# Performance work log

Hardware: AMD Instinct MI355X
Metric: run time of the kernel (lower is better)

Reference implementation:

```python
import jax, jax.numpy as jnp
import numpy as np

EPS = 1e-5
NEG_SLOPE = 0.2  # torch LeakyReLU default in DGCNN-style SharedMLPs


def knn_idx(p, k):
    # p: [B, 3, N]; returns idx [B, N, k] of k nearest neighbors (incl. self)
    inner = jnp.einsum('bdn,bdm->bnm', p, p)           # [B,N,N]
    sq = jnp.sum(p * p, axis=1)                         # [B,N]
    neg_dist = 2.0 * inner - sq[:, :, None] - sq[:, None, :]
    return jax.lax.top_k(neg_dist, k)[1]                # [B,N,k]


def smlp1d(x, w, b, g, bt):
    # x: [B,C,N]; 1x1 conv + BatchNorm1d (batch stats) + LeakyReLU
    y = jnp.einsum('bcn,oc->bon', x, w) + b[None, :, None]
    m = y.mean(axis=(0, 2), keepdims=True)
    v = y.var(axis=(0, 2), keepdims=True)
    y = g[None, :, None] * (y - m) * jax.lax.rsqrt(v + EPS) + bt[None, :, None]
    return jax.nn.leaky_relu(y, NEG_SLOPE)


def edgeconv(x, idx, w, b, g, bt):
    # x: [B,C,N], idx: [B,N,k] -> [B,O,N]
    B = x.shape[0]
    xT = jnp.transpose(x, (0, 2, 1))                    # [B,N,C]
    nb = xT[jnp.arange(B)[:, None, None], idx]          # [B,N,k,C] gather
    ctr = jnp.broadcast_to(xT[:, :, None, :], nb.shape)
    feat = jnp.concatenate([nb - ctr, ctr], axis=-1)    # [B,N,k,2C]
    y = jnp.einsum('bnkc,oc->bnko', feat, w) + b        # 1x1 conv2d
    m = y.mean(axis=(0, 1, 2), keepdims=True)
    v = y.var(axis=(0, 1, 2), keepdims=True)
    y = g * (y - m) * jax.lax.rsqrt(v + EPS) + bt
    y = jax.nn.leaky_relu(y, NEG_SLOPE)
    y = jnp.max(y, axis=2)                              # max over k -> [B,N,O]
    return jnp.transpose(y, (0, 2, 1))                  # [B,O,N]


def setup_inputs() -> dict:
    key = jax.random.key(0)
    ks = jax.random.split(key, 16)
    B, N, K = 2, 8192, 20
    C_in = 1024 + 3 * 64  # emb_dims + n_edgeconvs_backbone*64 = 1216
    OUT = 50

    def lin(k, o, c):
        return jax.random.normal(k, (o, c), jnp.float32) * (1.0 / np.sqrt(c))

    return {
        'x': jax.random.normal(ks[0], (B, C_in, N), jnp.float32),
        'p': jax.random.normal(ks[1], (B, 3, N), jnp.float32),
        # smlp1: 1216 -> 256
        'w1': lin(ks[2], 256, C_in), 'b1': jnp.zeros((256,), jnp.float32),
        'g1': jnp.ones((256,), jnp.float32), 'bt1': jnp.zeros((256,), jnp.float32),
        # edgeconv: 512 -> 256
        'we': lin(ks[3], 256, 512), 'be': jnp.zeros((256,), jnp.float32),
        'ge': jnp.ones((256,), jnp.float32), 'bte': jnp.zeros((256,), jnp.float32),
        # smlp2 part 1: 256 -> 256
        'w2': lin(ks[4], 256, 256), 'b2': jnp.zeros((256,), jnp.float32),
        'g2': jnp.ones((256,), jnp.float32), 'bt2': jnp.zeros((256,), jnp.float32),
        # smlp2 part 2: 256 -> 128
        'w3': lin(ks[5], 128, 256), 'b3': jnp.zeros((128,), jnp.float32),
        'g3': jnp.ones((128,), jnp.float32), 'bt3': jnp.zeros((128,), jnp.float32),
        # final conv1d: 128 -> 50
        'wf': lin(ks[6], OUT, 128), 'bf': jnp.zeros((OUT,), jnp.float32),
    }


def reference(x, p, w1, b1, g1, bt1, we, be, ge, bte,
              w2, b2, g2, bt2, w3, b3, g3, bt3, wf, bf):
    K = 20
    h = smlp1d(x, w1, b1, g1, bt1)              # [B,256,N]
    idx = knn_idx(p, K)                          # [B,N,K]
    h = edgeconv(h, idx, we, be, ge, bte)        # [B,256,N]
    h = smlp1d(h, w2, b2, g2, bt2)               # Dropout2d: identity (eval)
    h = smlp1d(h, w3, b3, g3, bt3)               # [B,128,N]
    return jnp.einsum('bcn,oc->bon', h, wf) + bf[None, :, None]  # [B,50,N]
```

## Files before the change

### kernel.cpp

```cpp
#include <hip/hip_runtime.h>

typedef unsigned short u16;
typedef unsigned int   u32;
typedef unsigned long long u64;
typedef __attribute__((ext_vector_type(4))) float f4;
typedef __attribute__((ext_vector_type(8))) short s8;
typedef __attribute__((ext_vector_type(4))) int   i4v;
typedef __attribute__((ext_vector_type(4))) unsigned short u16x4;

#define DEV __device__ __forceinline__

DEV u16 f2b(float f) {
  u32 u = __float_as_uint(f);
  return (u16)((u + 0x7FFFu + ((u >> 16) & 1u)) >> 16);
}
DEV float b2f(u16 h) { return __uint_as_float(((u32)h) << 16); }

#define OFF_STATS 0L
#define OFF_W1B   65536L
#define OFF_WEAB  688128L
#define OFF_W2B   950272L
#define OFF_W3B   1081344L
#define OFF_IDX   1146880L
#define OFF_PQ    2457600L
#define OFF_XT    4194304L
#define OFF_Y1    44040192L
#define OFF_Y2    4194304L
#define OFF_EMAX  23068672L
#define OFF_EMIN  41943040L
#define OFF_Y3    4194304L
#define OFF_Y4    23068672L
#define WS_NEED   71303168L

__global__ __launch_bounds__(256) void k_convw(
    const float* __restrict__ w1, const float* __restrict__ we,
    const float* __restrict__ w2, const float* __restrict__ w3,
    u16* __restrict__ w1b, u16* __restrict__ weABb,
    u16* __restrict__ w2b, u16* __restrict__ w3b)
{
  int i = blockIdx.x * 256 + threadIdx.x;
  if (i < 311296) { w1b[i] = f2b(w1[i]); return; }
  i -= 311296;
  if (i < 131072) {
    int o = i >> 8, c = i & 255;
    float v = (o < 256) ? we[o * 512 + c]
                        : we[(o - 256) * 512 + 256 + c] - we[(o - 256) * 512 + c];
    weABb[i] = f2b(v); return;
  }
  i -= 131072;
  if (i < 65536) { w2b[i] = f2b(w2[i]); return; }
  i -= 65536;
  if (i < 32768) { w3b[i] = f2b(w3[i]); }
}

__global__ __launch_bounds__(256) void k_prep(const float* __restrict__ p, f4* __restrict__ pqg)
{
  int i = blockIdx.x * 256 + threadIdx.x;
  int b = i >> 13, n = i & 8191;
  const float* pb = p + (long)b * 24576;
  float X = pb[n], Y = pb[8192 + n], Z = pb[16384 + n];
  f4 v; v[0] = X; v[1] = Y; v[2] = Z; v[3] = fmaf(X, X, fmaf(Y, Y, Z * Z));
  pqg[i] = v;
}

__global__ __launch_bounds__(256) void k_xt(const float* __restrict__ x, u16* __restrict__ xt)
{
  __shared__ float t[64][65];
  const int b = blockIdx.z, ct = blockIdx.y, nt = blockIdx.x;
  const int tx = threadIdx.x & 63, ty = threadIdx.x >> 6;
  const float* xb = x + (long)b * 1216 * 8192;
#pragma unroll
  for (int i = 0; i < 16; ++i) {
    int c = ct * 64 + ty + i * 4;
    t[ty + i * 4][tx] = xb[(long)c * 8192 + nt * 64 + tx];
  }
  __syncthreads();
  u16* xtb = xt + (long)b * 8192 * 1216;
#pragma unroll
  for (int i = 0; i < 16; ++i) {
    int n = nt * 64 + ty + i * 4;
    xtb[(long)n * 1216 + ct * 64 + tx] = f2b(t[tx][ty + i * 4]);
  }
}

__global__ __launch_bounds__(256) void k_knn(const f4* __restrict__ pqg, int* __restrict__ idxOut)
{
  __shared__ u16 cand[4][4][128];
  __shared__ double ckeyv[4][128];
  __shared__ int scnt[4][4];
  const int tid = threadIdx.x, lane = tid & 63, w = tid >> 6;
  const int blk = blockIdx.x;
  const int b = blk >> 9;
  const int qbase = ((blk & 511) << 4) + (w << 2);
  const f4* __restrict__ P = pqg + ((long)b << 13);
  if (lane < 4) scnt[w][lane] = 0;
  float qx2[4], qy2[4], qz2[4];
#pragma unroll
  for (int j = 0; j < 4; ++j) {
    f4 Q = P[qbase + j];
    qx2[j] = Q[0] + Q[0]; qy2[j] = Q[1] + Q[1]; qz2[j] = Q[2] + Q[2];
  }
  float mx[4];
#pragma unroll
  for (int j = 0; j < 4; ++j) mx[j] = -3.0e38f;
#pragma unroll 4
  for (int t = 0; t < 128; ++t) {
    f4 c = P[(t << 6) + lane];
#pragma unroll
    for (int j = 0; j < 4; ++j) {
      float v = fmaf(qx2[j], c[0], fmaf(qy2[j], c[1], fmaf(qz2[j], c[2], -c[3])));
      mx[j] = fmaxf(mx[j], v);
    }
  }
  float sv[4];
#pragma unroll
  for (int j = 0; j < 4; ++j) sv[j] = mx[j];
#pragma unroll
  for (int k = 2; k <= 64; k <<= 1) {
#pragma unroll
    for (int s = k >> 1; s > 0; s >>= 1) {
      const bool takeMin = (((lane & k) == 0) == ((lane & s) == 0));
#pragma unroll
      for (int j = 0; j < 4; ++j) {
        float o = __shfl_xor(sv[j], s);
        sv[j] = takeMin ? fminf(sv[j], o) : fmaxf(sv[j], o);
      }
    }
  }
  float T[4];
#pragma unroll
  for (int j = 0; j < 4; ++j) T[j] = __shfl(sv[j], 44) - 1e-3f;
  asm volatile("s_waitcnt lgkmcnt(0)" ::: "memory");
#pragma unroll 2
  for (int t = 0; t < 128; ++t) {
    f4 c = P[(t << 6) + lane];
#pragma unroll
    for (int j = 0; j < 4; ++j) {
      float v = fmaf(qx2[j], c[0], fmaf(qy2[j], c[1], fmaf(qz2[j], c[2], -c[3])));
      if (v >= T[j]) {
        int pos = atomicAdd(&scnt[w][j], 1);
        if (pos < 128) cand[w][j][pos] = (u16)((t << 6) + lane);
      }
    }
  }
  asm volatile("s_waitcnt lgkmcnt(0)" ::: "memory");
  for (int j = 0; j < 4; ++j) {
    int cn = scnt[w][j]; if (cn > 128) cn = 128;
    f4 Q = P[qbase + j];
    const double Qx = (double)Q[0], Qy = (double)Q[1], Qz = (double)Q[2];
    const double Qs = Qx * Qx + Qy * Qy + Qz * Qz;
    double myV[2]; int myI[2];
#pragma unroll
    for (int jj = 0; jj < 2; ++jj) {
      const int e = lane + (jj << 6);
      myV[jj] = -1.0e300; myI[jj] = 0x7FFFFFFF;
      if (e < cn) {
        const int ci = cand[w][j][e];
        f4 c = P[ci];
        double cx = (double)c[0], cy = (double)c[1], cz = (double)c[2];
        double v = 2.0 * (Qx * cx + Qy * cy + Qz * cz) - Qs - (cx * cx + cy * cy + cz * cz);
        myV[jj] = v; myI[jj] = ci;
        ckeyv[w][e] = v;
      }
    }
    asm volatile("s_waitcnt lgkmcnt(0)" ::: "memory");
    int rk0 = 0, rk1 = 0;
#pragma unroll 4
    for (int e2 = 0; e2 < cn; ++e2) {
      double ov = ckeyv[w][e2];
      int oi = (int)cand[w][j][e2];
      rk0 += ((ov > myV[0]) || (ov == myV[0] && oi < myI[0])) ? 1 : 0;
      rk1 += ((ov > myV[1]) || (ov == myV[1] && oi < myI[1])) ? 1 : 0;
    }
    int* orow = idxOut + (((long)b << 13) + qbase + j) * 20;
    if (lane < cn && rk0 < 20) orow[rk0] = myI[0];
    if (lane + 64 < cn && rk1 < 20) orow[rk1] = myI[1];
    asm volatile("s_waitcnt lgkmcnt(0)" ::: "memory");
  }
}

DEV float lky(float z) { return z > 0.f ? z : 0.2f * z; }

DEV i4v applyPack8(f4 a, f4 b4, const float* sc, const float* sh, int kb) {
  u16 r[8];
#pragma unroll
  for (int e = 0; e < 4; ++e) r[e] = f2b(lky(fmaf(sc[kb + e], a[e], sh[kb + e])));
#pragma unroll
  for (int e = 0; e < 4; ++e) r[4 + e] = f2b(lky(fmaf(sc[kb + 4 + e], b4[e], sh[kb + 4 + e])));
  i4v o;
#pragma unroll
  for (int e = 0; e < 4; ++e) o[e] = (int)((u32)r[2 * e] | ((u32)r[2 * e + 1] << 16));
  return o;
}

DEV i4v selPack8(f4 a, f4 b4, f4 a2, f4 b2, const float* sc, const float* sh, int kb) {
  u16 r[8];
#pragma unroll
  for (int e = 0; e < 4; ++e) {
    float s = sc[kb + e];
    float y = (s >= 0.f) ? a[e] : a2[e];
    r[e] = f2b(lky(fmaf(s, y, sh[kb + e])));
  }
#pragma unroll
  for (int e = 0; e < 4; ++e) {
    float s = sc[kb + 4 + e];
    float y = (s >= 0.f) ? b4[e] : b2[e];
    r[4 + e] = f2b(lky(fmaf(s, y, sh[kb + 4 + e])));
  }
  i4v o;
#pragma unroll
  for (int e = 0; e < 4; ++e) o[e] = (int)((u32)r[2 * e] | ((u32)r[2 * e + 1] << 16));
  return o;
}

template<int BMODE, int STATS, int BF16OUT>
__global__ __launch_bounds__(256, 2) void k_gemm(
    const u16* __restrict__ A, const void* __restrict__ B0v, const void* __restrict__ B1v,
    const float* __restrict__ sums, const float* __restrict__ ssq,
    const float* __restrict__ g, const float* __restrict__ bt, float invCount,
    float* __restrict__ gsums, float* __restrict__ gssq,
    void* __restrict__ Yv, int M, int K, long strideB, long strideY)
{
  __shared__ u16 sA[2][4096];
  __shared__ u16 sB[2][4096];
  __shared__ float scB[256], shB[256];
  __shared__ float s_sum[128], s_ssq[128];
  const int b = blockIdx.z;
  const int m0 = blockIdx.y * 128;
  const int n0 = blockIdx.x * 128;
  const int tid = threadIdx.x, lane = tid & 63, w = tid >> 6;
  const int wr = w >> 1, wc = w & 1;
  const int r15 = lane & 15, g8 = (lane >> 4) * 8;

  if (BMODE != 0) {
    float m = sums[tid] * invCount;
    float v = ssq[tid] * invCount - m * m;
    float s = g[tid] / sqrtf(v + 1e-5f);
    scB[tid] = s;
    shB[tid] = bt[tid] - m * s;
  }
  if (STATS) { if (tid < 128) { s_sum[tid] = 0.f; s_ssq[tid] = 0.f; } }
  if (BMODE != 0) __syncthreads();

  f4 acc[4][4];
#pragma unroll
  for (int i = 0; i < 4; ++i)
#pragma unroll
    for (int j = 0; j < 4; ++j) { f4 z = {0.f, 0.f, 0.f, 0.f}; acc[i][j] = z; }

  const int row0 = tid >> 2;
  const int kp0 = (tid & 3) << 3;
  const u16* gA0 = A + (long)(m0 + row0) * K + kp0;
  const u16* gA1 = A + (long)(m0 + row0 + 64) * K + kp0;
  const int ch0 = tid, ch1 = tid + 256;

  const u16* gB0 = (const u16*)B0v + (long)b * strideB + (long)(n0 + row0) * K + kp0;
  const u16* gB1 = gB0 + (long)64 * K;
  const float* fB0 = (const float*)B0v + (long)b * strideB + (long)(n0 + row0) * K + kp0;
  const float* fB1 = fB0 + (long)64 * K;
  const float* eB0 = (const float*)B1v + (long)b * strideB + (long)(n0 + row0) * K + kp0;
  const float* eB1 = eB0 + (long)64 * K;

  ((i4v*)sA[0])[ch0] = *(const i4v*)gA0;
  ((i4v*)sA[0])[ch1] = *(const i4v*)gA1;
  if (BMODE == 0) {
    ((i4v*)sB[0])[ch0] = *(const i4v*)gB0;
    ((i4v*)sB[0])[ch1] = *(const i4v*)gB1;
  } else if (BMODE == 1) {
    ((i4v*)sB[0])[ch0] = applyPack8(*(const f4*)fB0, *(const f4*)(fB0 + 4), scB, shB, kp0);
    ((i4v*)sB[0])[ch1] = applyPack8(*(const f4*)fB1, *(const f4*)(fB1 + 4), scB, shB, kp0);
  } else {
    ((i4v*)sB[0])[ch0] = selPack8(*(const f4*)fB0, *(const f4*)(fB0 + 4),
                                  *(const f4*)eB0, *(const f4*)(eB0 + 4), scB, shB, kp0);
    ((i4v*)sB[0])[ch1] = selPack8(*(const f4*)fB1, *(const f4*)(fB1 + 4),
                                  *(const f4*)eB1, *(const f4*)(eB1 + 4), scB, shB, kp0);
  }
  __syncthreads();

  const int KT = K >> 5;
  int cur = 0;
  for (int kk = 0; kk < KT; ++kk) {
    const bool more = (kk + 1 < KT);
    i4v ra0, ra1, rb0, rb1;
    f4 p0a, p0b, p1a, p1b, q0a, q0b, q1a, q1b;
    if (more) {
      long ko = (long)(kk + 1) * 32;
      ra0 = *(const i4v*)(gA0 + ko); ra1 = *(const i4v*)(gA1 + ko);
      if (BMODE == 0) {
        rb0 = *(const i4v*)(gB0 + ko); rb1 = *(const i4v*)(gB1 + ko);
      } else {
        p0a = *(const f4*)(fB0 + ko); p0b = *(const f4*)(fB0 + ko + 4);
        p1a = *(const f4*)(fB1 + ko); p1b = *(const f4*)(fB1 + ko + 4);
        if (BMODE == 2) {
          q0a = *(const f4*)(eB0 + ko); q0b = *(const f4*)(eB0 + ko + 4);
          q1a = *(const f4*)(eB1 + ko); q1b = *(const f4*)(eB1 + ko + 4);
        }
      }
    }
    const u16* la = sA[cur];
    const u16* lb = sB[cur];
    s8 af[4], bfr[4];
#pragma unroll
    for (int mi = 0; mi < 4; ++mi)
      af[mi] = *(const s8*)(la + (wr * 64 + mi * 16 + r15) * 32 + g8);
#pragma unroll
    for (int ni = 0; ni < 4; ++ni)
      bfr[ni] = *(const s8*)(lb + (wc * 64 + ni * 16 + r15) * 32 + g8);
#pragma unroll
    for (int mi = 0; mi < 4; ++mi)
#pragma unroll
      for (int ni = 0; ni < 4; ++ni)
        acc[mi][ni] = __builtin_amdgcn_mfma_f32_16x16x32_bf16(af[mi], bfr[ni], acc[mi][ni], 0, 0, 0);
    if (more) {
      ((i4v*)sA[cur ^ 1])[ch0] = ra0; ((i4v*)sA[cur ^ 1])[ch1] = ra1;
      if (BMODE == 0) {
        ((i4v*)sB[cur ^ 1])[ch0] = rb0; ((i4v*)sB[cur ^ 1])[ch1] = rb1;
      } else {
        const int kb = (kk + 1) * 32 + kp0;
        if (BMODE == 1) {
          ((i4v*)sB[cur ^ 1])[ch0] = applyPack8(p0a, p0b, scB, shB, kb);
          ((i4v*)sB[cur ^ 1])[ch1] = applyPack8(p1a, p1b, scB, shB, kb);
        } else {
          ((i4v*)sB[cur ^ 1])[ch0] = selPack8(p0a, p0b, q0a, q0b, scB, shB, kb);
          ((i4v*)sB[cur ^ 1])[ch1] = selPack8(p1a, p1b, q1a, q1b, scB, shB, kb);
        }
      }
    }
    __syncthreads();
    cur ^= 1;
  }
  const int og = m0 + wr * 64 + (lane >> 4) * 4;
  const int ng = n0 + wc * 64 + r15;
  if (BF16OUT) {
    u16* Yp = (u16*)Yv + (long)b * strideY;
#pragma unroll
    for (int mi = 0; mi < 4; ++mi)
#pragma unroll
      for (int ni = 0; ni < 4; ++ni) {
        f4 a = acc[mi][ni];
        u16x4 r;
#pragma unroll
        for (int q = 0; q < 4; ++q) r[q] = f2b(a[q]);
        *(u16x4*)(Yp + (long)(ng + ni * 16) * M + og + mi * 16) = r;
      }
  } else {
    float* Yp = (float*)Yv + (long)b * strideY;
#pragma unroll
    for (int mi = 0; mi < 4; ++mi)
#pragma unroll
      for (int ni = 0; ni < 4; ++ni)
        *(f4*)(Yp + (long)(ng + ni * 16) * M + og + mi * 16) = acc[mi][ni];
  }
  if (STATS) {
#pragma unroll
    for (int mi = 0; mi < 4; ++mi)
#pragma unroll
      for (int j = 0; j < 4; ++j) {
        float s = 0.f, q = 0.f;
#pragma unroll
        for (int ni = 0; ni < 4; ++ni) {
          float v = acc[mi][ni][j];
          s += v; q = fmaf(v, v, q);
        }
#pragma unroll
        for (int off = 1; off < 16; off <<= 1) {
          s += __shfl_xor(s, off);
          q += __shfl_xor(q, off);
        }
        if ((lane & 15) == 0) {
          int lc = wr * 64 + (lane >> 4) * 4 + mi * 16 + j;
          atomicAdd(&s_sum[lc], s);
          atomicAdd(&s_ssq[lc], q);
        }
      }
    __syncthreads();
    if (tid < 128) {
      atomicAdd(&gsums[m0 + tid], s_sum[tid]);
      atomicAdd(&gssq[m0 + tid], s_ssq[tid]);
    }
  }
}

__global__ __launch_bounds__(256, 2) void k_edge_gather(
    const u16* __restrict__ Y2, const int* __restrict__ idx,
    float* __restrict__ Emax, float* __restrict__ Emin,
    float* __restrict__ sums, float* __restrict__ ssq)
{
  __shared__ float s_sum[256], s_ssq[256];
  const int tid = threadIdx.x, lane = tid & 63, w = tid >> 6;
  s_sum[tid] = 0.f; s_ssq[tid] = 0.f;
  __syncthreads();
  const int ptBase = blockIdx.x * 64;
  f4 lsum = {0.f, 0.f, 0.f, 0.f}, lssq = {0.f, 0.f, 0.f, 0.f};
  for (int i = 0; i < 16; ++i) {
    const int pt = ptBase + w * 16 + i;
    const int b = pt >> 13;
    u16x4 cr = *(const u16x4*)(Y2 + (long)pt * 512 + 256 + (lane << 2));
    f4 ctr; ctr[0] = b2f(cr[0]); ctr[1] = b2f(cr[1]); ctr[2] = b2f(cr[2]); ctr[3] = b2f(cr[3]);
    const int* irow = idx + (long)pt * 20;
    f4 vmax = {-3.0e38f, -3.0e38f, -3.0e38f, -3.0e38f};
    f4 vmin = {3.0e38f, 3.0e38f, 3.0e38f, 3.0e38f};
#pragma unroll 4
    for (int k = 0; k < 20; ++k) {
      int m = irow[k];
      u16x4 nr = *(const u16x4*)(Y2 + (((long)b << 13) + m) * 512 + (lane << 2));
#pragma unroll
      for (int j = 0; j < 4; ++j) {
        float y = b2f(nr[j]) + ctr[j];
        vmax[j] = fmaxf(vmax[j], y);
        vmin[j] = fminf(vmin[j], y);
        lsum[j] += y;
        lssq[j] = fmaf(y, y, lssq[j]);
      }
    }
    *(f4*)(Emax + (long)pt * 256 + (lane << 2)) = vmax;
    *(f4*)(Emin + (long)pt * 256 + (lane << 2)) = vmin;
  }
#pragma unroll
  for (int j = 0; j < 4; ++j) {
    atomicAdd(&s_sum[(lane << 2) + j], lsum[j]);
    atomicAdd(&s_ssq[(lane << 2) + j], lssq[j]);
  }
  __syncthreads();
  atomicAdd(&sums[tid], s_sum[tid]);
  atomicAdd(&ssq[tid], s_ssq[tid]);
}

__global__ __launch_bounds__(64) void k_final(
    const float* __restrict__ Y4, const float* __restrict__ sums, const float* __restrict__ ssq,
    const float* __restrict__ g, const float* __restrict__ bt,
    const float* __restrict__ wf, const float* __restrict__ bf,
    float* __restrict__ out)
{
  __shared__ float swf[128][56];
  __shared__ float sc[128], sh[128], sb[52];
  const int lane = threadIdx.x;
  if (lane < 50) {
    const float* wrow = wf + lane * 128;
#pragma unroll 8
    for (int ch = 0; ch < 128; ++ch) swf[ch][lane] = wrow[ch];
    sb[lane] = bf[lane];
  } else if (lane < 52) {
#pragma unroll 8
    for (int ch = 0; ch < 128; ++ch) swf[ch][lane] = 0.f;
    sb[lane] = 0.f;
  }
#pragma unroll
  for (int t = 0; t < 2; ++t) {
    int ch = lane + t * 64;
    float m = sums[ch] * (1.0f / 16384.0f);
    float v = ssq[ch] * (1.0f / 16384.0f) - m * m;
    float s = g[ch] / sqrtf(v + 1e-5f);
    sc[ch] = s;
    sh[ch] = bt[ch] - m * s;
  }
  __syncthreads();
  const int b = blockIdx.y;
  const int n = blockIdx.x * 64 + lane;
  const float* hp = Y4 + ((long)b * 8192 + n) * 128;
  f4 av[13];
#pragma unroll
  for (int i = 0; i < 13; ++i) { f4 z = {0.f, 0.f, 0.f, 0.f}; av[i] = z; }
#pragma unroll 4
  for (int c4 = 0; c4 < 32; ++c4) {
    f4 hv = *(const f4*)(hp + c4 * 4);
#pragma unroll
    for (int e = 0; e < 4; ++e) {
      const int ch = c4 * 4 + e;
      float z = lky(fmaf(sc[ch], hv[e], sh[ch]));
#pragma unroll
      for (int o4 = 0; o4 < 13; ++o4) {
        f4 wv = *(const f4*)&swf[ch][o4 * 4];
#pragma unroll
        for (int q = 0; q < 4; ++q) av[o4][q] = fmaf(z, wv[q], av[o4][q]);
      }
    }
  }
  float* ob = out + (((long)b * 50) << 13) + n;
#pragma unroll
  for (int o4 = 0; o4 < 13; ++o4)
#pragma unroll
    for (int q = 0; q < 4; ++q) {
      int o = o4 * 4 + q;
      if (o < 50) ob[(long)o << 13] = av[o4][q] + sb[o];
    }
}

extern "C" void kernel_launch(void* const* d_in, const int* in_sizes, int n_in,
                              void* d_out, int out_size, void* d_ws, size_t ws_size,
                              hipStream_t stream)
{
  if ((long)ws_size < WS_NEED) return;
  const float* x   = (const float*)d_in[0];
  const float* p   = (const float*)d_in[1];
  const float* w1  = (const float*)d_in[2];
  const float* g1w = (const float*)d_in[4];
  const float* bt1 = (const float*)d_in[5];
  const float* we  = (const float*)d_in[6];
  const float* gew = (const float*)d_in[8];
  const float* bte = (const float*)d_in[9];
  const float* w2  = (const float*)d_in[10];
  const float* g2w = (const float*)d_in[12];
  const float* bt2 = (const float*)d_in[13];
  const float* w3  = (const float*)d_in[14];
  const float* g3w = (const float*)d_in[16];
  const float* bt3 = (const float*)d_in[17];
  const float* wf  = (const float*)d_in[18];
  const float* bfi = (const float*)d_in[19];

  char* ws = (char*)d_ws;
  u16* w1b   = (u16*)(ws + OFF_W1B);
  u16* weABb = (u16*)(ws + OFF_WEAB);
  u16* w2b   = (u16*)(ws + OFF_W2B);
  u16* w3b   = (u16*)(ws + OFF_W3B);
  int* idxb  = (int*)(ws + OFF_IDX);
  f4*  pqg   = (f4*)(ws + OFF_PQ);
  u16*   XT   = (u16*)(ws + OFF_XT);
  float* Y1   = (float*)(ws + OFF_Y1);
  u16*   Y2b  = (u16*)(ws + OFF_Y2);
  float* EMAX = (float*)(ws + OFF_EMAX);
  float* EMIN = (float*)(ws + OFF_EMIN);
  float* Y3   = (float*)(ws + OFF_Y3);
  float* Y4   = (float*)(ws + OFF_Y4);
  float* st0 = (float*)(ws + OFF_STATS);
  float* st1 = (float*)(ws + OFF_STATS + 4096);
  float* st2 = (float*)(ws + OFF_STATS + 8192);
  float* st3 = (float*)(ws + OFF_STATS + 12288);

  hipMemsetAsync(ws + OFF_STATS, 0, 16384, stream);
  k_convw<<<2112, 256, 0, stream>>>(w1, we, w2, w3, w1b, weABb, w2b, w3b);
  k_prep<<<64, 256, 0, stream>>>(p, pqg);
  k_knn<<<1024, 256, 0, stream>>>(pqg, idxb);
  k_xt<<<dim3(128, 19, 2), 256, 0, stream>>>(x, XT);

  k_gemm<0, 1, 0><<<dim3(64, 2, 2), 256, 0, stream>>>(
      w1b, XT, nullptr, nullptr, nullptr, nullptr, nullptr, 0.f,
      st0, st0 + 256, Y1, 256, 1216, (long)8192 * 1216, (long)8192 * 256);

  k_gemm<1, 0, 1><<<dim3(64, 4, 2), 256, 0, stream>>>(
      weABb, Y1, nullptr, st0, st0 + 256, g1w, bt1, 1.0f / 16384.0f,
      nullptr, nullptr, Y2b, 512, 256, (long)8192 * 256, (long)8192 * 512);

  k_edge_gather<<<256, 256, 0, stream>>>(Y2b, idxb, EMAX, EMIN, st1, st1 + 256);

  k_gemm<2, 1, 0><<<dim3(64, 2, 2), 256, 0, stream>>>(
      w2b, EMAX, EMIN, st1, st1 + 256, gew, bte, 1.0f / 327680.0f,
      st2, st2 + 256, Y3, 256, 256, (long)8192 * 256, (long)8192 * 256);

  k_gemm<1, 1, 0><<<dim3(64, 1, 2), 256, 0, stream>>>(
      w3b, Y3, nullptr, st2, st2 + 256, g2w, bt2, 1.0f / 16384.0f,
      st3, st3 + 256, Y4, 128, 256, (long)8192 * 256, (long)8192 * 128);

  k_final<<<dim3(128, 2), 64, 0, stream>>>(Y4, st3, st3 + 256, g3w, bt3, wf, bfi, (float*)d_out);
}
```

Measured before the change: 259.2 us.

## Stage kNN points in LDS, store edge max/min as bf16, split gather over channels

Measured after the change: 235.5 us. 9.1% less time.

```diff
diff --git a/kernel.cpp b/kernel.cpp
--- a/kernel.cpp
+++ b/kernel.cpp
@@ -85,6 +85,7 @@
 
 __global__ __launch_bounds__(256) void k_knn(const f4* __restrict__ pqg, int* __restrict__ idxOut)
 {
+  __shared__ f4 chunk[1024];
   __shared__ u16 cand[4][4][128];
   __shared__ double ckeyv[4][128];
   __shared__ int scnt[4][4];
@@ -103,13 +104,19 @@
   float mx[4];
 #pragma unroll
   for (int j = 0; j < 4; ++j) mx[j] = -3.0e38f;
-#pragma unroll 4
-  for (int t = 0; t < 128; ++t) {
-    f4 c = P[(t << 6) + lane];
-#pragma unroll
-    for (int j = 0; j < 4; ++j) {
-      float v = fmaf(qx2[j], c[0], fmaf(qy2[j], c[1], fmaf(qz2[j], c[2], -c[3])));
-      mx[j] = fmaxf(mx[j], v);
+  for (int c = 0; c < 8; ++c) {
+    __syncthreads();
+#pragma unroll
+    for (int i = 0; i < 4; ++i) chunk[tid + i * 256] = P[c * 1024 + tid + i * 256];
+    __syncthreads();
+#pragma unroll 2
+    for (int t = 0; t < 16; ++t) {
+      f4 cc = chunk[(t << 6) + lane];
+#pragma unroll
+      for (int j = 0; j < 4; ++j) {
+        float v = fmaf(qx2[j], cc[0], fmaf(qy2[j], cc[1], fmaf(qz2[j], cc[2], -cc[3])));
+        mx[j] = fmaxf(mx[j], v);
+      }
     }
   }
   float sv[4];
@@ -130,16 +137,21 @@
   float T[4];
 #pragma unroll
   for (int j = 0; j < 4; ++j) T[j] = __shfl(sv[j], 44) - 1e-3f;
-  asm volatile("s_waitcnt lgkmcnt(0)" ::: "memory");
+  for (int c = 0; c < 8; ++c) {
+    __syncthreads();
+#pragma unroll
+    for (int i = 0; i < 4; ++i) chunk[tid + i * 256] = P[c * 1024 + tid + i * 256];
+    __syncthreads();
 #pragma unroll 2
-  for (int t = 0; t < 128; ++t) {
-    f4 c = P[(t << 6) + lane];
-#pragma unroll
-    for (int j = 0; j < 4; ++j) {
-      float v = fmaf(qx2[j], c[0], fmaf(qy2[j], c[1], fmaf(qz2[j], c[2], -c[3])));
-      if (v >= T[j]) {
-        int pos = atomicAdd(&scnt[w][j], 1);
-        if (pos < 128) cand[w][j][pos] = (u16)((t << 6) + lane);
+    for (int t = 0; t < 16; ++t) {
+      f4 cc = chunk[(t << 6) + lane];
+#pragma unroll
+      for (int j = 0; j < 4; ++j) {
+        float v = fmaf(qx2[j], cc[0], fmaf(qy2[j], cc[1], fmaf(qz2[j], cc[2], -cc[3])));
+        if (v >= T[j]) {
+          int pos = atomicAdd(&scnt[w][j], 1);
+          if (pos < 128) cand[w][j][pos] = (u16)(c * 1024 + (t << 6) + lane);
+        }
       }
     }
   }
@@ -193,19 +205,16 @@
   return o;
 }
 
-DEV i4v selPack8(f4 a, f4 b4, f4 a2, f4 b2, const float* sc, const float* sh, int kb) {
+DEV i4v selPack8b(i4v rawM, i4v rawN, const float* sc, const float* sh, int kb) {
   u16 r[8];
 #pragma unroll
-  for (int e = 0; e < 4; ++e) {
+  for (int e = 0; e < 8; ++e) {
+    u32 dM = (u32)rawM[e >> 1], dN = (u32)rawN[e >> 1];
+    u16 hM = (e & 1) ? (u16)(dM >> 16) : (u16)(dM & 0xFFFFu);
+    u16 hN = (e & 1) ? (u16)(dN >> 16) : (u16)(dN & 0xFFFFu);
     float s = sc[kb + e];
-    float y = (s >= 0.f) ? a[e] : a2[e];
+    float y = (s >= 0.f) ? b2f(hM) : b2f(hN);
     r[e] = f2b(lky(fmaf(s, y, sh[kb + e])));
-  }
-#pragma unroll
-  for (int e = 0; e < 4; ++e) {
-    float s = sc[kb + 4 + e];
-    float y = (s >= 0.f) ? b4[e] : b2[e];
-    r[4 + e] = f2b(lky(fmaf(s, y, sh[kb + 4 + e])));
   }
   i4v o;
 #pragma unroll
@@ -258,8 +267,8 @@
   const u16* gB1 = gB0 + (long)64 * K;
   const float* fB0 = (const float*)B0v + (long)b * strideB + (long)(n0 + row0) * K + kp0;
   const float* fB1 = fB0 + (long)64 * K;
-  const float* eB0 = (const float*)B1v + (long)b * strideB + (long)(n0 + row0) * K + kp0;
-  const float* eB1 = eB0 + (long)64 * K;
+  const u16* nB0 = (const u16*)B1v + (long)b * strideB + (long)(n0 + row0) * K + kp0;
+  const u16* nB1 = nB0 + (long)64 * K;
 
   ((i4v*)sA[0])[ch0] = *(const i4v*)gA0;
   ((i4v*)sA[0])[ch1] = *(const i4v*)gA1;
@@ -270,10 +279,8 @@
     ((i4v*)sB[0])[ch0] = applyPack8(*(const f4*)fB0, *(const f4*)(fB0 + 4), scB, shB, kp0);
     ((i4v*)sB[0])[ch1] = applyPack8(*(const f4*)fB1, *(const f4*)(fB1 + 4), scB, shB, kp0);
   } else {
-    ((i4v*)sB[0])[ch0] = selPack8(*(const f4*)fB0, *(const f4*)(fB0 + 4),
-                                  *(const f4*)eB0, *(const f4*)(eB0 + 4), scB, shB, kp0);
-    ((i4v*)sB[0])[ch1] = selPack8(*(const f4*)fB1, *(const f4*)(fB1 + 4),
-                                  *(const f4*)eB1, *(const f4*)(eB1 + 4), scB, shB, kp0);
+    ((i4v*)sB[0])[ch0] = selPack8b(*(const i4v*)gB0, *(const i4v*)nB0, scB, shB, kp0);
+    ((i4v*)sB[0])[ch1] = selPack8b(*(const i4v*)gB1, *(const i4v*)nB1, scB, shB, kp0);
   }
   __syncthreads();
 
@@ -281,20 +288,19 @@
   int cur = 0;
   for (int kk = 0; kk < KT; ++kk) {
     const bool more = (kk + 1 < KT);
-    i4v ra0, ra1, rb0, rb1;
-    f4 p0a, p0b, p1a, p1b, q0a, q0b, q1a, q1b;
+    i4v ra0, ra1, rb0, rb1, rn0, rn1;
+    f4 p0a, p0b, p1a, p1b;
     if (more) {
       long ko = (long)(kk + 1) * 32;
       ra0 = *(const i4v*)(gA0 + ko); ra1 = *(const i4v*)(gA1 + ko);
       if (BMODE == 0) {
         rb0 = *(const i4v*)(gB0 + ko); rb1 = *(const i4v*)(gB1 + ko);
-      } else {
+      } else if (BMODE == 1) {
         p0a = *(const f4*)(fB0 + ko); p0b = *(const f4*)(fB0 + ko + 4);
         p1a = *(const f4*)(fB1 + ko); p1b = *(const f4*)(fB1 + ko + 4);
-        if (BMODE == 2) {
-          q0a = *(const f4*)(eB0 + ko); q0b = *(const f4*)(eB0 + ko + 4);
-          q1a = *(const f4*)(eB1 + ko); q1b = *(const f4*)(eB1 + ko + 4);
-        }
+      } else {
+        rb0 = *(const i4v*)(gB0 + ko); rb1 = *(const i4v*)(gB1 + ko);
+        rn0 = *(const i4v*)(nB0 + ko); rn1 = *(const i4v*)(nB1 + ko);
       }
     }
     const u16* la = sA[cur];
@@ -315,15 +321,14 @@
       ((i4v*)sA[cur ^ 1])[ch0] = ra0; ((i4v*)sA[cur ^ 1])[ch1] = ra1;
       if (BMODE == 0) {
         ((i4v*)sB[cur ^ 1])[ch0] = rb0; ((i4v*)sB[cur ^ 1])[ch1] = rb1;
+      } else if (BMODE == 1) {
+        const int kb = (kk + 1) * 32 + kp0;
+        ((i4v*)sB[cur ^ 1])[ch0] = applyPack8(p0a, p0b, scB, shB, kb);
+        ((i4v*)sB[cur ^ 1])[ch1] = applyPack8(p1a, p1b, scB, shB, kb);
       } else {
         const int kb = (kk + 1) * 32 + kp0;
-        if (BMODE == 1) {
-          ((i4v*)sB[cur ^ 1])[ch0] = applyPack8(p0a, p0b, scB, shB, kb);
-          ((i4v*)sB[cur ^ 1])[ch1] = applyPack8(p1a, p1b, scB, shB, kb);
-        } else {
-          ((i4v*)sB[cur ^ 1])[ch0] = selPack8(p0a, p0b, q0a, q0b, scB, shB, kb);
-          ((i4v*)sB[cur ^ 1])[ch1] = selPack8(p1a, p1b, q1a, q1b, scB, shB, kb);
-        }
+        ((i4v*)sB[cur ^ 1])[ch0] = selPack8b(rb0, rn0, scB, shB, kb);
+        ((i4v*)sB[cur ^ 1])[ch1] = selPack8b(rb1, rn1, scB, shB, kb);
       }
     }
     __syncthreads();
@@ -383,27 +388,30 @@
 
 __global__ __launch_bounds__(256, 2) void k_edge_gather(
     const u16* __restrict__ Y2, const int* __restrict__ idx,
-    float* __restrict__ Emax, float* __restrict__ Emin,
+    u16* __restrict__ Emax, u16* __restrict__ Emin,
     float* __restrict__ sums, float* __restrict__ ssq)
 {
   __shared__ float s_sum[256], s_ssq[256];
   const int tid = threadIdx.x, lane = tid & 63, w = tid >> 6;
   s_sum[tid] = 0.f; s_ssq[tid] = 0.f;
   __syncthreads();
-  const int ptBase = blockIdx.x * 64;
+  const int half = blockIdx.y, b = blockIdx.z;
+  const int ptBase = blockIdx.x * 64 + w * 16;
+  const int sub = lane >> 5;
+  const int chOff = half * 128 + ((lane & 31) << 2);
   f4 lsum = {0.f, 0.f, 0.f, 0.f}, lssq = {0.f, 0.f, 0.f, 0.f};
-  for (int i = 0; i < 16; ++i) {
-    const int pt = ptBase + w * 16 + i;
-    const int b = pt >> 13;
-    u16x4 cr = *(const u16x4*)(Y2 + (long)pt * 512 + 256 + (lane << 2));
+  for (int i = 0; i < 8; ++i) {
+    const int pt = ptBase + i * 2 + sub;
+    const long gp = (long)b * 8192 + pt;
+    u16x4 cr = *(const u16x4*)(Y2 + gp * 512 + 256 + chOff);
     f4 ctr; ctr[0] = b2f(cr[0]); ctr[1] = b2f(cr[1]); ctr[2] = b2f(cr[2]); ctr[3] = b2f(cr[3]);
-    const int* irow = idx + (long)pt * 20;
+    const int* irow = idx + gp * 20;
     f4 vmax = {-3.0e38f, -3.0e38f, -3.0e38f, -3.0e38f};
     f4 vmin = {3.0e38f, 3.0e38f, 3.0e38f, 3.0e38f};
 #pragma unroll 4
     for (int k = 0; k < 20; ++k) {
       int m = irow[k];
-      u16x4 nr = *(const u16x4*)(Y2 + (((long)b << 13) + m) * 512 + (lane << 2));
+      u16x4 nr = *(const u16x4*)(Y2 + ((long)b * 8192 + m) * 512 + chOff);
 #pragma unroll
       for (int j = 0; j < 4; ++j) {
         float y = b2f(nr[j]) + ctr[j];
@@ -413,13 +421,16 @@
         lssq[j] = fmaf(y, y, lssq[j]);
       }
     }
-    *(f4*)(Emax + (long)pt * 256 + (lane << 2)) = vmax;
-    *(f4*)(Emin + (long)pt * 256 + (lane << 2)) = vmin;
+    u16x4 eM, eN;
+#pragma unroll
+    for (int j = 0; j < 4; ++j) { eM[j] = f2b(vmax[j]); eN[j] = f2b(vmin[j]); }
+    *(u16x4*)(Emax + gp * 256 + chOff) = eM;
+    *(u16x4*)(Emin + gp * 256 + chOff) = eN;
   }
 #pragma unroll
   for (int j = 0; j < 4; ++j) {
-    atomicAdd(&s_sum[(lane << 2) + j], lsum[j]);
-    atomicAdd(&s_ssq[(lane << 2) + j], lssq[j]);
+    atomicAdd(&s_sum[chOff + j], lsum[j]);
+    atomicAdd(&s_ssq[chOff + j], lssq[j]);
   }
   __syncthreads();
   atomicAdd(&sums[tid], s_sum[tid]);
@@ -518,8 +529,8 @@
   u16*   XT   = (u16*)(ws + OFF_XT);
   float* Y1   = (float*)(ws + OFF_Y1);
   u16*   Y2b  = (u16*)(ws + OFF_Y2);
-  float* EMAX = (float*)(ws + OFF_EMAX);
-  float* EMIN = (float*)(ws + OFF_EMIN);
+  u16*   EMAX = (u16*)(ws + OFF_EMAX);
+  u16*   EMIN = (u16*)(ws + OFF_EMIN);
   float* Y3   = (float*)(ws + OFF_Y3);
   float* Y4   = (float*)(ws + OFF_Y4);
   float* st0 = (float*)(ws + OFF_STATS);
@@ -541,7 +552,7 @@
       weABb, Y1, nullptr, st0, st0 + 256, g1w, bt1, 1.0f / 16384.0f,
       nullptr, nullptr, Y2b, 512, 256, (long)8192 * 256, (long)8192 * 512);
 
-  k_edge_gather<<<256, 256, 0, stream>>>(Y2b, idxb, EMAX, EMIN, st1, st1 + 256);
+  k_edge_gather<<<dim3(128, 2, 2), 256, 0, stream>>>(Y2b, idxb, EMAX, EMIN, st1, st1 + 256);
 
   k_gemm<2, 1, 0><<<dim3(64, 2, 2), 256, 0, stream>>>(
       w2b, EMAX, EMIN, st1, st1 + 256, gew, bte, 1.0f / 327680.0f,
```
